# Optimization experiments

Measured on AMD Instinct MI355X. Metric: run time of the kernel, lower is better.

Reference implementation:

```python
import jax, jax.numpy as jnp
import numpy as np
import math

EPS = 1e-12  # F.normalize default eps

def _l2_normalize(x):
    n = jnp.sqrt(jnp.sum(x * x, axis=-1, keepdims=True))
    return x / jnp.maximum(n, EPS)

def setup_inputs() -> dict:
    key = jax.random.key(0)
    k1, k2 = jax.random.split(key)
    B, F, C = 16384, 1024, 1000
    features = jax.random.normal(k1, (B, F), dtype=jnp.float32)
    prototypes = jax.random.normal(k2, (C, F), dtype=jnp.float32)
    distance_scale = jnp.ones((1,), dtype=jnp.float32)
    temperature = jnp.ones((1,), dtype=jnp.float32)
    return {"features": features, "prototypes": prototypes,
            "distance_scale": distance_scale, "temperature": temperature}

def reference(features, prototypes, distance_scale, temperature):
    # L2-normalize both sides (F.normalize, p=2, eps=1e-12)
    f = _l2_normalize(features)      # [B, F]
    p = _l2_normalize(prototypes)    # [C, F]
    # Pairwise Euclidean distance. For unit vectors ||f-p||^2 = 2 - 2 f.p,
    # clamped at 0 for numerical safety; then / sqrt(2).
    sim = jnp.einsum('bf,cf->bc', f, p)                  # [B, C]
    sq = jnp.maximum(2.0 - 2.0 * sim, 0.0)
    distances = jnp.sqrt(sq) / jnp.float32(math.sqrt(2.0))
    iso = jnp.abs(distance_scale) * distances            # [B, C]
    logits = -(iso + jnp.mean(iso, axis=1, keepdims=True))
    return logits / temperature
```

## Files before the change

kernel.cpp:

```cpp
#include <hip/hip_runtime.h>
#include <hip/hip_cooperative_groups.h>
#include <hip/hip_bf16.h>
#include <math.h>

#define B_ROWS 16384
#define C_COLS 1000
#define C_PAD  1024
#define FDIM   1024
#define FBLKS  4096
#define FP8_SCALE 256.0f
#define INV_SIM   (1.0f / (FP8_SCALE * FP8_SCALE))

typedef __attribute__((ext_vector_type(8))) short bf16x8;
typedef __attribute__((ext_vector_type(4))) float f32x4;
typedef __attribute__((ext_vector_type(4))) int   i32x4;
typedef __attribute__((ext_vector_type(8))) int   i32x8;

#define GLD_LDS(gp, lp) __builtin_amdgcn_global_load_lds( \
    (__attribute__((address_space(1))) void*)(gp),        \
    (__attribute__((address_space(3))) void*)(lp), 16, 0, 0)

__global__ __launch_bounds__(256) void normalize_all(
    const float* __restrict__ feat, const float* __restrict__ prot,
    unsigned char* __restrict__ fb, unsigned char* __restrict__ pb,
    float* __restrict__ rowsum)
{
    const int lane = threadIdx.x & 63;
    const int wave = threadIdx.x >> 6;

    if (blockIdx.x < 64) rowsum[blockIdx.x * 256 + threadIdx.x] = 0.0f;

    const float* in;
    unsigned char* out;
    int row, nvalid;
    if (blockIdx.x < FBLKS) {
        row = blockIdx.x * 4 + wave;  in = feat; out = fb; nvalid = B_ROWS;
    } else {
        row = (blockIdx.x - FBLKS) * 4 + wave;  in = prot; out = pb; nvalid = C_COLS;
    }
    unsigned char* orow = out + (size_t)row * FDIM;

    if (row >= nvalid) {
        i32x4 z = {0, 0, 0, 0};
        ((i32x4*)orow)[lane] = z;
        return;
    }

    const float4* rp = (const float4*)(in + (size_t)row * FDIM);
    float4 v[4];
    float ss = 0.0f;
    #pragma unroll
    for (int c = 0; c < 4; ++c) {
        v[c] = rp[lane * 4 + c];
        ss += v[c].x * v[c].x + v[c].y * v[c].y + v[c].z * v[c].z + v[c].w * v[c].w;
    }
    #pragma unroll
    for (int off = 1; off < 64; off <<= 1) ss += __shfl_xor(ss, off, 64);
    const float inv = FP8_SCALE / sqrtf(fmaxf(ss, 1e-24f));

    i32x4 pk;
    #pragma unroll
    for (int c = 0; c < 4; ++c) {
        int w0 = __builtin_amdgcn_cvt_pk_fp8_f32(v[c].x * inv, v[c].y * inv, 0, false);
        w0     = __builtin_amdgcn_cvt_pk_fp8_f32(v[c].z * inv, v[c].w * inv, w0, true);
        pk[c] = w0;
    }
    ((i32x4*)orow)[lane] = pk;
}

__global__ __launch_bounds__(256, 4) void gemm_dist_out(
    const unsigned char* __restrict__ A,
    const unsigned char* __restrict__ Bp,
    float* __restrict__ rowsum,
    const float* __restrict__ scale,
    const float* __restrict__ temp,
    float* __restrict__ out)
{
    __shared__ unsigned char As[128 * 128];
    __shared__ unsigned char Bs[128 * 128];

    const int tid  = threadIdx.x;
    const int lane = tid & 63;
    const int wave = tid >> 6;

    const int id  = blockIdx.x;
    const int xcd = id & 7;
    const int seq = id >> 3;
    const int bn  = seq & 7;
    const int bm  = xcd * 16 + (seq >> 3);

    const int waveM = (wave >> 1) * 64;
    const int waveN = (wave & 1) * 64;

    f32x4 acc[4][4] = {};

    const int srow8 = lane >> 3;
    const int sg    = (lane & 7) ^ srow8;
    const unsigned char* Abase = A  + ((size_t)(bm * 128 + wave * 8 + srow8)) * FDIM + sg * 16;
    const unsigned char* Bbase = Bp + ((size_t)(bn * 128 + wave * 8 + srow8)) * FDIM + sg * 16;

    const int q2   = (lane >> 4) * 2;
    const int bxor = lane & 7;
    const int fA = (waveM + (lane & 15)) * 128;
    const int fB = (waveN + (lane & 15)) * 128;
    const int pg0 = ((q2)     ^ bxor) * 16;
    const int pg1 = ((q2 + 1) ^ bxor) * 16;

    #pragma unroll 1
    for (int k0 = 0; k0 < FDIM; k0 += 128) {
        __syncthreads();
        #pragma unroll
        for (int r = 0; r < 4; ++r) {
            GLD_LDS(Abase + (size_t)(r * 32) * FDIM + k0, &As[(r * 32 + wave * 8) * 128]);
            GLD_LDS(Bbase + (size_t)(r * 32) * FDIM + k0, &Bs[(r * 32 + wave * 8) * 128]);
        }
        __syncthreads();

        i32x8 b[4];
        #pragma unroll
        for (int nt = 0; nt < 4; ++nt) {
            const i32x4 lo = *(const i32x4*)&Bs[fB + nt * 2048 + pg0];
            const i32x4 hi = *(const i32x4*)&Bs[fB + nt * 2048 + pg1];
            b[nt] = (i32x8){lo.x, lo.y, lo.z, lo.w, hi.x, hi.y, hi.z, hi.w};
        }
        #pragma unroll
        for (int mt = 0; mt < 4; ++mt) {
            const i32x4 lo = *(const i32x4*)&As[fA + mt * 2048 + pg0];
            const i32x4 hi = *(const i32x4*)&As[fA + mt * 2048 + pg1];
            const i32x8 a = (i32x8){lo.x, lo.y, lo.z, lo.w, hi.x, hi.y, hi.z, hi.w};
            #pragma unroll
            for (int nt = 0; nt < 4; ++nt)
                acc[mt][nt] = __builtin_amdgcn_mfma_scale_f32_16x16x128_f8f6f4(
                    a, b[nt], acc[mt][nt], 0, 0, 0, 127, 0, 127);
        }
    }

    const int row0 = bm * 128 + waveM;
    const int col0 = bn * 128 + waveN;
    #pragma unroll
    for (int mt = 0; mt < 4; ++mt) {
        #pragma unroll
        for (int r = 0; r < 4; ++r) {
            float part = 0.0f;
            #pragma unroll
            for (int nt = 0; nt < 4; ++nt) {
                const float sim = acc[mt][nt][r] * INV_SIM;
                const float dv = sqrtf(fmaxf(1.0f - sim, 0.0f));
                acc[mt][nt][r] = dv;
                const int col = col0 + nt * 16 + (lane & 15);
                if (col < C_COLS) part += dv;
            }
            part += __shfl_xor(part, 1, 64);
            part += __shfl_xor(part, 2, 64);
            part += __shfl_xor(part, 4, 64);
            part += __shfl_xor(part, 8, 64);
            if ((lane & 15) == 0)
                atomicAdd(&rowsum[row0 + mt * 16 + (lane >> 4) * 4 + r], part);
        }
    }

    cooperative_groups::this_grid().sync();

    const float aS = -fabsf(scale[0]) / temp[0];
    #pragma unroll
    for (int mt = 0; mt < 4; ++mt) {
        #pragma unroll
        for (int r = 0; r < 4; ++r) {
            const int row = row0 + mt * 16 + (lane >> 4) * 4 + r;
            const float m = __hip_atomic_load(&rowsum[row], __ATOMIC_RELAXED,
                                              __HIP_MEMORY_SCOPE_AGENT) * (1.0f / (float)C_COLS);
            #pragma unroll
            for (int nt = 0; nt < 4; ++nt) {
                const int col = col0 + nt * 16 + (lane & 15);
                if (col < C_COLS)
                    out[(size_t)row * C_COLS + col] = aS * (acc[mt][nt][r] + m);
            }
        }
    }
}

__global__ __launch_bounds__(256) void gemm_dist(
    const unsigned char* __restrict__ A,
    const unsigned char* __restrict__ Bp,
    __hip_bfloat16* __restrict__ D,
    float* __restrict__ rowsum)
{
    __shared__ unsigned char As[128 * 128];
    __shared__ unsigned char Bs[128 * 128];

    const int tid  = threadIdx.x;
    const int lane = tid & 63;
    const int wave = tid >> 6;

    const int id  = blockIdx.x;
    const int xcd = id & 7;
    const int seq = id >> 3;
    const int bn  = seq & 7;
    const int bm  = xcd * 16 + (seq >> 3);

    const int waveM = (wave >> 1) * 64;
    const int waveN = (wave & 1) * 64;

    f32x4 acc[4][4] = {};

    const int srow8 = lane >> 3;
    const int sg    = (lane & 7) ^ srow8;
    const unsigned char* Abase = A  + ((size_t)(bm * 128 + wave * 8 + srow8)) * FDIM + sg * 16;
    const unsigned char* Bbase = Bp + ((size_t)(bn * 128 + wave * 8 + srow8)) * FDIM + sg * 16;

    const int q2   = (lane >> 4) * 2;
    const int bxor = lane & 7;
    const int fA = (waveM + (lane & 15)) * 128;
    const int fB = (waveN + (lane & 15)) * 128;
    const int pg0 = ((q2)     ^ bxor) * 16;
    const int pg1 = ((q2 + 1) ^ bxor) * 16;

    #pragma unroll 1
    for (int k0 = 0; k0 < FDIM; k0 += 128) {
        __syncthreads();
        #pragma unroll
        for (int r = 0; r < 4; ++r) {
            GLD_LDS(Abase + (size_t)(r * 32) * FDIM + k0, &As[(r * 32 + wave * 8) * 128]);
            GLD_LDS(Bbase + (size_t)(r * 32) * FDIM + k0, &Bs[(r * 32 + wave * 8) * 128]);
        }
        __syncthreads();

        i32x8 b[4];
        #pragma unroll
        for (int nt = 0; nt < 4; ++nt) {
            const i32x4 lo = *(const i32x4*)&Bs[fB + nt * 2048 + pg0];
            const i32x4 hi = *(const i32x4*)&Bs[fB + nt * 2048 + pg1];
            b[nt] = (i32x8){lo.x, lo.y, lo.z, lo.w, hi.x, hi.y, hi.z, hi.w};
        }
        #pragma unroll
        for (int mt = 0; mt < 4; ++mt) {
            const i32x4 lo = *(const i32x4*)&As[fA + mt * 2048 + pg0];
            const i32x4 hi = *(const i32x4*)&As[fA + mt * 2048 + pg1];
            const i32x8 a = (i32x8){lo.x, lo.y, lo.z, lo.w, hi.x, hi.y, hi.z, hi.w};
            #pragma unroll
            for (int nt = 0; nt < 4; ++nt)
                acc[mt][nt] = __builtin_amdgcn_mfma_scale_f32_16x16x128_f8f6f4(
                    a, b[nt], acc[mt][nt], 0, 0, 0, 127, 0, 127);
        }
    }

    const int row0 = bm * 128 + waveM;
    const int col0 = bn * 128 + waveN;
    #pragma unroll
    for (int mt = 0; mt < 4; ++mt) {
        #pragma unroll
        for (int r = 0; r < 4; ++r) {
            const int row = row0 + mt * 16 + (lane >> 4) * 4 + r;
            float part = 0.0f;
            #pragma unroll
            for (int nt = 0; nt < 4; ++nt) {
                const int col = col0 + nt * 16 + (lane & 15);
                const float sim = acc[mt][nt][r] * INV_SIM;
                const float dv = sqrtf(fmaxf(1.0f - sim, 0.0f));
                if (col < C_COLS) {
                    D[(size_t)row * C_COLS + col] = __float2bfloat16(dv);
                    part += dv;
                }
            }
            part += __shfl_xor(part, 1, 64);
            part += __shfl_xor(part, 2, 64);
            part += __shfl_xor(part, 4, 64);
            part += __shfl_xor(part, 8, 64);
            if ((lane & 15) == 0) atomicAdd(&rowsum[row], part);
        }
    }
}

__global__ __launch_bounds__(256) void finalize(
    const __hip_bfloat16* __restrict__ D, const float* __restrict__ rowsum,
    const float* __restrict__ scale, const float* __restrict__ temp,
    float* __restrict__ out)
{
    const size_t i = (size_t)blockIdx.x * 256 + threadIdx.x;
    const float a = -fabsf(scale[0]) / temp[0];
    const int row = (int)((i * 8) / C_COLS);
    const float m = rowsum[row] * (1.0f / (float)C_COLS);

    const bf16x8 dv = *(const bf16x8*)(D + i * 8);
    const __hip_bfloat16* dp = (const __hip_bfloat16*)&dv;
    float4 o0, o1;
    o0.x = a * (__bfloat162float(dp[0]) + m);
    o0.y = a * (__bfloat162float(dp[1]) + m);
    o0.z = a * (__bfloat162float(dp[2]) + m);
    o0.w = a * (__bfloat162float(dp[3]) + m);
    o1.x = a * (__bfloat162float(dp[4]) + m);
    o1.y = a * (__bfloat162float(dp[5]) + m);
    o1.z = a * (__bfloat162float(dp[6]) + m);
    o1.w = a * (__bfloat162float(dp[7]) + m);
    ((float4*)out)[i * 2]     = o0;
    ((float4*)out)[i * 2 + 1] = o1;
}

extern "C" void kernel_launch(void* const* d_in, const int* in_sizes, int n_in,
                              void* d_out, int out_size, void* d_ws, size_t ws_size,
                              hipStream_t stream)
{
    const float* features = (const float*)d_in[0];
    const float* protos   = (const float*)d_in[1];
    const float* dscale   = (const float*)d_in[2];
    const float* temp     = (const float*)d_in[3];
    float* out = (float*)d_out;

    char* ws = (char*)d_ws;
    unsigned char* fb = (unsigned char*)ws;
    unsigned char* pb = (unsigned char*)(ws + 16777216);
    __hip_bfloat16* D = (__hip_bfloat16*)(ws + 17825792);
    float* rowsum     = (float*)(ws + 50593792);

    normalize_all<<<FBLKS + C_PAD / 4, 256, 0, stream>>>(features, protos, fb, pb, rowsum);

    static int use_coop = -1;
    if (use_coop < 0) {
        int dev = 0;
        (void)hipGetDevice(&dev);
        int coopOK = 0;
        (void)hipDeviceGetAttribute(&coopOK, hipDeviceAttributeCooperativeLaunch, dev);
        int numCU = 0;
        (void)hipDeviceGetAttribute(&numCU, hipDeviceAttributeMultiprocessorCount, dev);
        int maxB = 0;
        hipError_t oe = hipOccupancyMaxActiveBlocksPerMultiprocessor(
            &maxB, reinterpret_cast<const void*>(gemm_dist_out), 256, 0);
        use_coop = (coopOK && oe == hipSuccess && numCU > 0 &&
                    (long)maxB * numCU >= 1024) ? 1 : 0;
    }

    if (use_coop) {
        const unsigned char* gA = fb;
        const unsigned char* gB = pb;
        float* gR = rowsum;
        const float* gS = dscale;
        const float* gT = temp;
        float* gO = out;
        void* kargs[] = { (void*)&gA, (void*)&gB, (void*)&gR,
                          (void*)&gS, (void*)&gT, (void*)&gO };
        hipError_t le = hipLaunchCooperativeKernel(
            reinterpret_cast<const void*>(gemm_dist_out),
            dim3(1024), dim3(256), kargs, 0, stream);
        if (le != hipSuccess) use_coop = 0;
    }
    if (!use_coop) {
        gemm_dist<<<1024, 256, 0, stream>>>(fb, pb, D, rowsum);
        finalize<<<(B_ROWS * C_COLS / 8) / 256, 256, 0, stream>>>(D, rowsum, dscale, temp, out);
    }
}
```

Before: 160.7 us.

## Process two row tiles per cooperative block, holding the first tile in packed bf16

The cooperative fused kernel now launches 512 blocks instead of 1024, and each block computes two 128x128 output tiles one after the other. The distances of the first tile are packed to bf16 and kept in registers across the grid sync, while the second tile stays in fp32. After the sync, both tiles are written out with the row mean applied. The aim is to need fewer co-resident blocks for the grid-wide sync and to free registers from the 4-blocks-per-CU launch bound. In exchange, concurrency per CU is halved with no overlap between the two tiles, and the first tile loses precision by being rounded to bf16.

```diff
diff --git a/kernel.cpp b/kernel.cpp
--- a/kernel.cpp
+++ b/kernel.cpp
@@ -20,6 +20,20 @@
     (__attribute__((address_space(1))) void*)(gp),        \
     (__attribute__((address_space(3))) void*)(lp), 16, 0, 0)
 
+static __device__ __forceinline__ unsigned int pack2bf(float a, float b) {
+    __hip_bfloat16 ha = __float2bfloat16(a), hb = __float2bfloat16(b);
+    unsigned short ua, ub;
+    __builtin_memcpy(&ua, &ha, 2);
+    __builtin_memcpy(&ub, &hb, 2);
+    return (unsigned int)ua | ((unsigned int)ub << 16);
+}
+static __device__ __forceinline__ float unpackbf(unsigned int w, int hi) {
+    unsigned short us = (unsigned short)(hi ? (w >> 16) : (w & 0xffff));
+    __hip_bfloat16 h;
+    __builtin_memcpy(&h, &us, 2);
+    return __bfloat162float(h);
+}
+
 __global__ __launch_bounds__(256) void normalize_all(
     const float* __restrict__ feat, const float* __restrict__ prot,
     unsigned char* __restrict__ fb, unsigned char* __restrict__ pb,
@@ -68,7 +82,39 @@
     ((i32x4*)orow)[lane] = pk;
 }
 
-__global__ __launch_bounds__(256, 4) void gemm_dist_out(
+#define GEMM_TILE(BM_, BN_, ACC) do {                                                        \
+    const unsigned char* Abase_ = A  + ((size_t)((BM_) * 128 + wave * 8 + srow8)) * FDIM + sg * 16; \
+    const unsigned char* Bbase_ = Bp + ((size_t)((BN_) * 128 + wave * 8 + srow8)) * FDIM + sg * 16; \
+    _Pragma("unroll 1")                                                                      \
+    for (int k0_ = 0; k0_ < FDIM; k0_ += 128) {                                              \
+        __syncthreads();                                                                     \
+        _Pragma("unroll")                                                                    \
+        for (int r_ = 0; r_ < 4; ++r_) {                                                     \
+            GLD_LDS(Abase_ + (size_t)(r_ * 32) * FDIM + k0_, &As[(r_ * 32 + wave * 8) * 128]); \
+            GLD_LDS(Bbase_ + (size_t)(r_ * 32) * FDIM + k0_, &Bs[(r_ * 32 + wave * 8) * 128]); \
+        }                                                                                    \
+        __syncthreads();                                                                     \
+        i32x8 bfr_[4];                                                                       \
+        _Pragma("unroll")                                                                    \
+        for (int nt_ = 0; nt_ < 4; ++nt_) {                                                  \
+            const i32x4 lo_ = *(const i32x4*)&Bs[fB + nt_ * 2048 + pg0];                     \
+            const i32x4 hi_ = *(const i32x4*)&Bs[fB + nt_ * 2048 + pg1];                     \
+            bfr_[nt_] = (i32x8){lo_.x, lo_.y, lo_.z, lo_.w, hi_.x, hi_.y, hi_.z, hi_.w};     \
+        }                                                                                    \
+        _Pragma("unroll")                                                                    \
+        for (int mt_ = 0; mt_ < 4; ++mt_) {                                                  \
+            const i32x4 lo_ = *(const i32x4*)&As[fA + mt_ * 2048 + pg0];                     \
+            const i32x4 hi_ = *(const i32x4*)&As[fA + mt_ * 2048 + pg1];                     \
+            const i32x8 a_ = (i32x8){lo_.x, lo_.y, lo_.z, lo_.w, hi_.x, hi_.y, hi_.z, hi_.w};\
+            _Pragma("unroll")                                                                \
+            for (int nt_ = 0; nt_ < 4; ++nt_)                                                \
+                ACC[mt_][nt_] = __builtin_amdgcn_mfma_scale_f32_16x16x128_f8f6f4(            \
+                    a_, bfr_[nt_], ACC[mt_][nt_], 0, 0, 0, 127, 0, 127);                     \
+        }                                                                                    \
+    }                                                                                        \
+} while (0)
+
+__global__ __launch_bounds__(256) void gemm2_dist_out(
     const unsigned char* __restrict__ A,
     const unsigned char* __restrict__ Bp,
     float* __restrict__ rowsum,
@@ -87,18 +133,14 @@
     const int xcd = id & 7;
     const int seq = id >> 3;
     const int bn  = seq & 7;
-    const int bm  = xcd * 16 + (seq >> 3);
+    const int bm0 = xcd * 16 + (seq >> 3);
+    const int bm1 = bm0 + 8;
 
     const int waveM = (wave >> 1) * 64;
     const int waveN = (wave & 1) * 64;
 
-    f32x4 acc[4][4] = {};
-
     const int srow8 = lane >> 3;
     const int sg    = (lane & 7) ^ srow8;
-    const unsigned char* Abase = A  + ((size_t)(bm * 128 + wave * 8 + srow8)) * FDIM + sg * 16;
-    const unsigned char* Bbase = Bp + ((size_t)(bn * 128 + wave * 8 + srow8)) * FDIM + sg * 16;
-
     const int q2   = (lane >> 4) * 2;
     const int bxor = lane & 7;
     const int fA = (waveM + (lane & 15)) * 128;
@@ -106,74 +148,102 @@
     const int pg0 = ((q2)     ^ bxor) * 16;
     const int pg1 = ((q2 + 1) ^ bxor) * 16;
 
-    #pragma unroll 1
-    for (int k0 = 0; k0 < FDIM; k0 += 128) {
-        __syncthreads();
+    const int col0 = bn * 128 + waveN;
+
+    unsigned int pk1[4][4][2];
+    {
+        f32x4 acc[4][4] = {};
+        GEMM_TILE(bm0, bn, acc);
+
+        const int row0 = bm0 * 128 + waveM;
+        #pragma unroll
+        for (int mt = 0; mt < 4; ++mt) {
+            #pragma unroll
+            for (int r = 0; r < 4; ++r) {
+                float part = 0.0f;
+                #pragma unroll
+                for (int nt = 0; nt < 4; ++nt) {
+                    const float sim = acc[mt][nt][r] * INV_SIM;
+                    const float dv = sqrtf(fmaxf(1.0f - sim, 0.0f));
+                    acc[mt][nt][r] = dv;
+                    const int col = col0 + nt * 16 + (lane & 15);
+                    if (col < C_COLS) part += dv;
+                }
+                part += __shfl_xor(part, 1, 64);
+                part += __shfl_xor(part, 2, 64);
+                part += __shfl_xor(part, 4, 64);
+                part += __shfl_xor(part, 8, 64);
+                if ((lane & 15) == 0)
+                    atomicAdd(&rowsum[row0 + mt * 16 + (lane >> 4) * 4 + r], part);
+            }
+            #pragma unroll
+            for (int nt = 0; nt < 4; ++nt) {
+                pk1[mt][nt][0] = pack2bf(acc[mt][nt][0], acc[mt][nt][1]);
+                pk1[mt][nt][1] = pack2bf(acc[mt][nt][2], acc[mt][nt][3]);
+            }
+        }
+    }
+
+    f32x4 acc2[4][4] = {};
+    GEMM_TILE(bm1, bn, acc2);
+    {
+        const int row0 = bm1 * 128 + waveM;
+        #pragma unroll
+        for (int mt = 0; mt < 4; ++mt) {
+            #pragma unroll
+            for (int r = 0; r < 4; ++r) {
+                float part = 0.0f;
+                #pragma unroll
+                for (int nt = 0; nt < 4; ++nt) {
+                    const float sim = acc2[mt][nt][r] * INV_SIM;
+                    const float dv = sqrtf(fmaxf(1.0f - sim, 0.0f));
+                    acc2[mt][nt][r] = dv;
+                    const int col = col0 + nt * 16 + (lane & 15);
+                    if (col < C_COLS) part += dv;
+                }
+                part += __shfl_xor(part, 1, 64);
+                part += __shfl_xor(part, 2, 64);
+                part += __shfl_xor(part, 4, 64);
+                part += __shfl_xor(part, 8, 64);
+                if ((lane & 15) == 0)
+                    atomicAdd(&rowsum[row0 + mt * 16 + (lane >> 4) * 4 + r], part);
+            }
+        }
+    }
+
+    cooperative_groups::this_grid().sync();
+
+    const float aS = -fabsf(scale[0]) / temp[0];
+
+    #pragma unroll
+    for (int mt = 0; mt < 4; ++mt) {
         #pragma unroll
         for (int r = 0; r < 4; ++r) {
-            GLD_LDS(Abase + (size_t)(r * 32) * FDIM + k0, &As[(r * 32 + wave * 8) * 128]);
-            GLD_LDS(Bbase + (size_t)(r * 32) * FDIM + k0, &Bs[(r * 32 + wave * 8) * 128]);
-        }
-        __syncthreads();
-
-        i32x8 b[4];
-        #pragma unroll
-        for (int nt = 0; nt < 4; ++nt) {
-            const i32x4 lo = *(const i32x4*)&Bs[fB + nt * 2048 + pg0];
-            const i32x4 hi = *(const i32x4*)&Bs[fB + nt * 2048 + pg1];
-            b[nt] = (i32x8){lo.x, lo.y, lo.z, lo.w, hi.x, hi.y, hi.z, hi.w};
-        }
-        #pragma unroll
-        for (int mt = 0; mt < 4; ++mt) {
-            const i32x4 lo = *(const i32x4*)&As[fA + mt * 2048 + pg0];
-            const i32x4 hi = *(const i32x4*)&As[fA + mt * 2048 + pg1];
-            const i32x8 a = (i32x8){lo.x, lo.y, lo.z, lo.w, hi.x, hi.y, hi.z, hi.w};
-            #pragma unroll
-            for (int nt = 0; nt < 4; ++nt)
-                acc[mt][nt] = __builtin_amdgcn_mfma_scale_f32_16x16x128_f8f6f4(
-                    a, b[nt], acc[mt][nt], 0, 0, 0, 127, 0, 127);
-        }
-    }
-
-    const int row0 = bm * 128 + waveM;
-    const int col0 = bn * 128 + waveN;
-    #pragma unroll
-    for (int mt = 0; mt < 4; ++mt) {
-        #pragma unroll
-        for (int r = 0; r < 4; ++r) {
-            float part = 0.0f;
-            #pragma unroll
-            for (int nt = 0; nt < 4; ++nt) {
-                const float sim = acc[mt][nt][r] * INV_SIM;
-                const float dv = sqrtf(fmaxf(1.0f - sim, 0.0f));
-                acc[mt][nt][r] = dv;
-                const int col = col0 + nt * 16 + (lane & 15);
-                if (col < C_COLS) part += dv;
-            }
-            part += __shfl_xor(part, 1, 64);
-            part += __shfl_xor(part, 2, 64);
-            part += __shfl_xor(part, 4, 64);
-            part += __shfl_xor(part, 8, 64);
-            if ((lane & 15) == 0)
-                atomicAdd(&rowsum[row0 + mt * 16 + (lane >> 4) * 4 + r], part);
-        }
-    }
-
-    cooperative_groups::this_grid().sync();
-
-    const float aS = -fabsf(scale[0]) / temp[0];
-    #pragma unroll
-    for (int mt = 0; mt < 4; ++mt) {
-        #pragma unroll
-        for (int r = 0; r < 4; ++r) {
-            const int row = row0 + mt * 16 + (lane >> 4) * 4 + r;
+            const int row = bm1 * 128 + waveM + mt * 16 + (lane >> 4) * 4 + r;
             const float m = __hip_atomic_load(&rowsum[row], __ATOMIC_RELAXED,
                                               __HIP_MEMORY_SCOPE_AGENT) * (1.0f / (float)C_COLS);
             #pragma unroll
             for (int nt = 0; nt < 4; ++nt) {
                 const int col = col0 + nt * 16 + (lane & 15);
                 if (col < C_COLS)
-                    out[(size_t)row * C_COLS + col] = aS * (acc[mt][nt][r] + m);
+                    out[(size_t)row * C_COLS + col] = aS * (acc2[mt][nt][r] + m);
+            }
+        }
+    }
+    #pragma unroll
+    for (int mt = 0; mt < 4; ++mt) {
+        #pragma unroll
+        for (int r = 0; r < 4; ++r) {
+            const int row = bm0 * 128 + waveM + mt * 16 + (lane >> 4) * 4 + r;
+            const float m = __hip_atomic_load(&rowsum[row], __ATOMIC_RELAXED,
+                                              __HIP_MEMORY_SCOPE_AGENT) * (1.0f / (float)C_COLS);
+            #pragma unroll
+            for (int nt = 0; nt < 4; ++nt) {
+                const int col = col0 + nt * 16 + (lane & 15);
+                if (col < C_COLS) {
+                    const float dv = unpackbf(pk1[mt][nt][r >> 1], r & 1);
+                    out[(size_t)row * C_COLS + col] = aS * (dv + m);
+                }
             }
         }
     }
@@ -205,9 +275,6 @@
 
     const int srow8 = lane >> 3;
     const int sg    = (lane & 7) ^ srow8;
-    const unsigned char* Abase = A  + ((size_t)(bm * 128 + wave * 8 + srow8)) * FDIM + sg * 16;
-    const unsigned char* Bbase = Bp + ((size_t)(bn * 128 + wave * 8 + srow8)) * FDIM + sg * 16;
-
     const int q2   = (lane >> 4) * 2;
     const int bxor = lane & 7;
     const int fA = (waveM + (lane & 15)) * 128;
@@ -215,34 +282,7 @@
     const int pg0 = ((q2)     ^ bxor) * 16;
     const int pg1 = ((q2 + 1) ^ bxor) * 16;
 
-    #pragma unroll 1
-    for (int k0 = 0; k0 < FDIM; k0 += 128) {
-        __syncthreads();
-        #pragma unroll
-        for (int r = 0; r < 4; ++r) {
-            GLD_LDS(Abase + (size_t)(r * 32) * FDIM + k0, &As[(r * 32 + wave * 8) * 128]);
-            GLD_LDS(Bbase + (size_t)(r * 32) * FDIM + k0, &Bs[(r * 32 + wave * 8) * 128]);
-        }
-        __syncthreads();
-
-        i32x8 b[4];
-        #pragma unroll
-        for (int nt = 0; nt < 4; ++nt) {
-            const i32x4 lo = *(const i32x4*)&Bs[fB + nt * 2048 + pg0];
-            const i32x4 hi = *(const i32x4*)&Bs[fB + nt * 2048 + pg1];
-            b[nt] = (i32x8){lo.x, lo.y, lo.z, lo.w, hi.x, hi.y, hi.z, hi.w};
-        }
-        #pragma unroll
-        for (int mt = 0; mt < 4; ++mt) {
-            const i32x4 lo = *(const i32x4*)&As[fA + mt * 2048 + pg0];
-            const i32x4 hi = *(const i32x4*)&As[fA + mt * 2048 + pg1];
-            const i32x8 a = (i32x8){lo.x, lo.y, lo.z, lo.w, hi.x, hi.y, hi.z, hi.w};
-            #pragma unroll
-            for (int nt = 0; nt < 4; ++nt)
-                acc[mt][nt] = __builtin_amdgcn_mfma_scale_f32_16x16x128_f8f6f4(
-                    a, b[nt], acc[mt][nt], 0, 0, 0, 127, 0, 127);
-        }
-    }
+    GEMM_TILE(bm, bn, acc);
 
     const int row0 = bm * 128 + waveM;
     const int col0 = bn * 128 + waveN;
@@ -324,9 +364,9 @@
         (void)hipDeviceGetAttribute(&numCU, hipDeviceAttributeMultiprocessorCount, dev);
         int maxB = 0;
         hipError_t oe = hipOccupancyMaxActiveBlocksPerMultiprocessor(
-            &maxB, reinterpret_cast<const void*>(gemm_dist_out), 256, 0);
+            &maxB, reinterpret_cast<const void*>(gemm2_dist_out), 256, 0);
         use_coop = (coopOK && oe == hipSuccess && numCU > 0 &&
-                    (long)maxB * numCU >= 1024) ? 1 : 0;
+                    (long)maxB * numCU >= 512) ? 1 : 0;
     }
 
     if (use_coop) {
@@ -339,8 +379,8 @@
         void* kargs[] = { (void*)&gA, (void*)&gB, (void*)&gR,
                           (void*)&gS, (void*)&gT, (void*)&gO };
         hipError_t le = hipLaunchCooperativeKernel(
-            reinterpret_cast<const void*>(gemm_dist_out),
-            dim3(1024), dim3(256), kargs, 0, stream);
+            reinterpret_cast<const void*>(gemm2_dist_out),
+            dim3(512), dim3(256), kargs, 0, stream);
         if (le != hipSuccess) use_coop = 0;
     }
     if (!use_coop) {
```

Measured after the change: 159.0 us. Within noise of the previous version (-1.1%).
